# Kernel tuning notes

Measured on AMD Instinct MI355X. Metric: run time of the kernel, lower is better.

Reference implementation:

```python
import jax, jax.numpy as jnp
import numpy as np

B, L, C, S, W, R = 2, 32, 32, 64, 64, 32
MH = 32  # forcing MLP hidden


def _conv3d(x, w, b, pad_hw):
    # x: [B, Cin, L, S, W], w: [Cout, Cin, 1, kh, kw]
    y = jax.lax.conv_general_dilated(
        x, w, window_strides=(1, 1, 1),
        padding=[(0, 0), (pad_hw, pad_hw), (pad_hw, pad_hw)],
        dimension_numbers=('NCDHW', 'OIDHW', 'NCDHW'))
    return y + b[None, :, None, None, None]


def _forward(x, listT, params_log_base, dispersion_mod, fm_W1, fm_b1, fm_W2, fm_b2,
             forcing_scale, U_re, U_im, V_re, V_im, pW_re, pW_im, pb_re, pb_im,
             convr_w, convr_b, convi_w, convi_b, projc_w, projc_b, ln_w, ln_b):
    b, l, c, s, w = x.shape
    r = U_re.shape[-1]
    pad = s // 4
    dt = listT.reshape(b, l, 1, 1, 1)

    # FFT with mirror padding along S
    xp = jnp.pad(x, ((0, 0), (0, 0), (0, 0), (pad, pad), (0, 0)), mode='reflect')
    h = jnp.fft.fft2(xp.astype(jnp.complex64), axes=(-2, -1), norm='ortho')

    # complex channel projection
    proj_W = pW_re + 1j * pW_im
    h = jnp.einsum('blcsw,cd->bldsw', h, proj_W)
    h = h + (pb_re + 1j * pb_im)[None, None, :, None, None]

    # back to spatial, crop pad, re-FFT
    hs = jnp.fft.ifft2(h, axes=(-2, -1), norm='ortho')[..., pad:-pad, :]
    h = jnp.fft.fft2(hs, axes=(-2, -1), norm='ortho')

    U = U_re + 1j * U_im          # [C, S, R]
    V = V_re + 1j * V_im          # [C, W, R]
    # zq[b,l,c,r,q] = sum_{s,w} h * conj(U)[c,s,r] * V[c,w,q]
    zq = jnp.einsum('blcsw,csr,cwq->blcrq', h, jnp.conj(U), V)

    nu_base = jnp.exp(params_log_base[0] + dispersion_mod[0]).reshape(1, 1, c, r, 1)
    th_base = jnp.exp(params_log_base[1] + dispersion_mod[1]).reshape(1, 1, c, r, 1)

    # forcing modulation
    ctx = x.mean(axis=(-2, -1))                       # [B, L, C]
    inp = jnp.concatenate([ctx, dt.reshape(b, l, 1)], axis=-1)
    mid = jnp.tanh(inp @ fm_W1 + fm_b1)
    mod = (mid @ fm_W2 + fm_b2).reshape(b, l, c, r, 2)
    dnu = (forcing_scale * jnp.tanh(mod[..., 0]))[..., None]
    dth = (forcing_scale * jnp.tanh(mod[..., 1]))[..., None]

    nu_t = jnp.maximum(nu_base * dt + dnu, 1e-6)       # [B, L, C, R, 1]
    th_t = th_base * dt + dth
    lamb = jnp.exp(jax.lax.complex(-nu_t, th_t))       # complex [B, L, C, R, 1]

    gamma = jnp.sqrt(jnp.maximum(1.0 - jnp.exp(-2.0 * nu_t), 1e-12))
    x_in = zq * gamma.astype(zq.dtype)                 # [B, L, C, R, R]

    # parallel linear-recurrence scan: z_t = lamb_t * z_{t-1} + x_t
    def comb(a, bb):
        a1, x1 = a
        a2, x2 = bb
        return a1 * a2, a2 * x1 + x2
    _, z_out = jax.lax.associative_scan(comb, (lamb, x_in), axis=1)

    # reconstruct spectral field and inverse FFT
    h_rec = jnp.einsum('blcrq,cwq,csr->blcsw', z_out, jnp.conj(V), U)
    h_sp = jnp.fft.ifft2(h_rec, axes=(-2, -1), norm='ortho')

    xr = jnp.transpose(h_sp.real, (0, 2, 1, 3, 4))     # [B, C, L, S, W]
    xi = jnp.transpose(h_sp.imag, (0, 2, 1, 3, 4))
    hr = _conv3d(xr, convr_w, convr_b, 1)
    hi = _conv3d(xi, convi_w, convi_b, 1)
    hf = _conv3d(jnp.concatenate([hr, hi], axis=1), projc_w, projc_b, 0)
    hf = jnp.transpose(hf, (0, 2, 1, 3, 4))            # [B, L, C, S, W]

    # LayerNorm over [S, W]
    mu = hf.mean(axis=(-2, -1), keepdims=True)
    var = hf.var(axis=(-2, -1), keepdims=True)
    hf = (hf - mu) / jnp.sqrt(var + 1e-5) * ln_w + ln_b

    return x + hf


def setup_inputs() -> dict:
    key = jax.random.key(0)
    ks = jax.random.split(key, 20)
    f32 = jnp.float32
    x = jax.random.normal(ks[0], (B, L, C, S, W), dtype=f32)
    listT = jax.random.uniform(ks[1], (B, L), dtype=f32, minval=0.5, maxval=1.5)

    r_min, r_max = 0.8, 0.99
    u1 = jax.random.uniform(ks[2], (C, R), dtype=f32)
    u2 = jax.random.uniform(ks[3], (C, R), dtype=f32)
    nu_log = jnp.log(-0.5 * jnp.log(u1 * (r_max ** 2 - r_min ** 2) + r_min ** 2))
    theta_log = jnp.log(u2 * (2.0 * np.pi))
    params_log_base = jnp.stack([nu_log, theta_log], axis=0)
    dispersion_mod = jnp.zeros((2, C, R), dtype=f32)

    fm_W1 = jax.random.normal(ks[4], (C + 1, MH), dtype=f32) / np.sqrt(C + 1)
    fm_b1 = jnp.zeros((MH,), dtype=f32)
    fm_W2 = jax.random.normal(ks[5], (MH, C * R * 2), dtype=f32) / np.sqrt(MH)
    fm_b2 = jnp.zeros((C * R * 2,), dtype=f32)
    forcing_scale = jnp.float32(0.1)

    cplx_scale = 1.0 / np.sqrt(2.0)
    U_re = jax.random.normal(ks[6], (C, S, R), dtype=f32) * cplx_scale / np.sqrt(S)
    U_im = jax.random.normal(ks[7], (C, S, R), dtype=f32) * cplx_scale / np.sqrt(S)
    V_re = jax.random.normal(ks[8], (C, W, R), dtype=f32) * cplx_scale / np.sqrt(W)
    V_im = jax.random.normal(ks[9], (C, W, R), dtype=f32) * cplx_scale / np.sqrt(W)
    pW_re = jax.random.normal(ks[10], (C, C), dtype=f32) * cplx_scale / np.sqrt(C)
    pW_im = jax.random.normal(ks[11], (C, C), dtype=f32) * cplx_scale / np.sqrt(C)
    pb_re = jnp.zeros((C,), dtype=f32)
    pb_im = jnp.zeros((C,), dtype=f32)

    convr_w = jax.random.normal(ks[12], (C, C, 1, 3, 3), dtype=f32) * (1.0 / np.sqrt(C * 9))
    convr_b = jnp.zeros((C,), dtype=f32)
    convi_w = jax.random.normal(ks[13], (C, C, 1, 3, 3), dtype=f32) * (1.0 / np.sqrt(C * 9))
    convi_b = jnp.zeros((C,), dtype=f32)
    projc_w = jax.random.normal(ks[14], (C, 2 * C, 1, 1, 1), dtype=f32) * (1.0 / np.sqrt(2 * C))
    projc_b = jnp.zeros((C,), dtype=f32)

    ln_w = jnp.ones((S, W), dtype=f32)
    ln_b = jnp.zeros((S, W), dtype=f32)

    return dict(x=x, listT=listT, params_log_base=params_log_base,
                dispersion_mod=dispersion_mod, fm_W1=fm_W1, fm_b1=fm_b1,
                fm_W2=fm_W2, fm_b2=fm_b2, forcing_scale=forcing_scale,
                U_re=U_re, U_im=U_im, V_re=V_re, V_im=V_im,
                pW_re=pW_re, pW_im=pW_im, pb_re=pb_re, pb_im=pb_im,
                convr_w=convr_w, convr_b=convr_b, convi_w=convi_w, convi_b=convi_b,
                projc_w=projc_w, projc_b=projc_b, ln_w=ln_w, ln_b=ln_b)


def reference(x, listT, params_log_base, dispersion_mod, fm_W1, fm_b1, fm_W2, fm_b2,
              forcing_scale, U_re, U_im, V_re, V_im, pW_re, pW_im, pb_re, pb_im,
              convr_w, convr_b, convi_w, convi_b, projc_w, projc_b, ln_w, ln_b):
    return _forward(x, listT, params_log_base, dispersion_mod, fm_W1, fm_b1, fm_W2,
                    fm_b2, forcing_scale, U_re, U_im, V_re, V_im, pW_re, pW_im,
                    pb_re, pb_im, convr_w, convr_b, convi_w, convi_b, projc_w,
                    projc_b, ln_w, ln_b)
```

## Files before the change

### kernel.cpp

```cpp
#include <hip/hip_runtime.h>


typedef __attribute__((ext_vector_type(8))) short short8;
typedef __attribute__((ext_vector_type(4))) float floatx4;

__device__ __forceinline__ unsigned pack_bf16(float re, float im) {
  unsigned a = __float_as_uint(re), b = __float_as_uint(im);
  a = (a + 0x7FFFu + ((a >> 16) & 1u)) >> 16;
  b = (b + 0x7FFFu + ((b >> 16) & 1u)) >> 16;
  return a | (b << 16);
}
__device__ __forceinline__ unsigned short bf16r(float v) {
  unsigned a = __float_as_uint(v);
  return (unsigned short)((a + 0x7FFFu + ((a >> 16) & 1u)) >> 16);
}

__global__ __launch_bounds__(256) void k_mixprep(
    const float* __restrict__ x, const float* __restrict__ pWr,
    const float* __restrict__ pWi,
    const float* __restrict__ U_re, const float* __restrict__ U_im,
    const float* __restrict__ V_re, const float* __restrict__ V_im,
    const float* __restrict__ projc_w, const float* __restrict__ convr_w,
    const float* __restrict__ convi_w,
    unsigned* __restrict__ hs, float* __restrict__ ctxp,
    unsigned* __restrict__ zqA, unsigned* __restrict__ recA,
    unsigned* __restrict__ recB, unsigned* __restrict__ Wtb) {
  __shared__ __align__(16) char smem[33280];
  const int tid = threadIdx.x;
  if (blockIdx.x < 1024) {
    unsigned* xb_s = (unsigned*)smem;
    float(*red)[16][2] = (float(*)[16][2])(smem + 20480);
    unsigned* outb = (unsigned*)smem;
    const int bl = blockIdx.x >> 4;
    const int seg = blockIdx.x & 15;
    const int pxbase = seg * 256;
    const float* xb = x + (size_t)bl * 131072 + pxbase;
    float csa = 0.f, csb = 0.f;
#pragma unroll
    for (int t = 0; t < 4; ++t) {
      int i = t * 256 + tid;
      int c2 = i & 15, g4 = i >> 4;
      float4 a = *(const float4*)(xb + (2 * c2) * 4096 + g4 * 4);
      float4 b = *(const float4*)(xb + (2 * c2 + 1) * 4096 + g4 * 4);
      csa += a.x + a.y + a.z + a.w;
      csb += b.x + b.y + b.z + b.w;
#pragma unroll
      for (int j = 0; j < 4; ++j) {
        int px = g4 * 4 + j;
        xb_s[px * 20 + (((c2 >> 2) ^ (px & 3)) << 2) + (c2 & 3)] =
            pack_bf16(((const float*)&a)[j], ((const float*)&b)[j]);
      }
    }
    red[tid & 15][tid >> 4][0] = csa;
    red[tid & 15][tid >> 4][1] = csb;
    const int lane = tid & 63, wv = tid >> 6;
    const int qd = lane >> 4, ln = lane & 15;
    short8 arL, aiL, arH, aiH;
#pragma unroll
    for (int j = 0; j < 8; ++j) {
      int ci = qd * 8 + j;
      ((short*)&arL)[j] = (short)bf16r(pWr[ci * 32 + ln]);
      ((short*)&aiL)[j] = (short)bf16r(pWi[ci * 32 + ln]);
      ((short*)&arH)[j] = (short)bf16r(pWr[ci * 32 + 16 + ln]);
      ((short*)&aiH)[j] = (short)bf16r(pWi[ci * 32 + 16 + ln]);
    }
    __syncthreads();
    if (tid < 32) {
      int c2 = tid >> 1, part = tid & 1;
      float s = 0.f;
#pragma unroll
      for (int w = 0; w < 16; ++w) s += red[c2][w][part];
      ctxp[(bl * 16 + seg) * 32 + 2 * c2 + part] = s;
    }
    floatx4 RL[4], IL[4], RH[4], IH[4];
#pragma unroll
    for (int pt = 0; pt < 4; ++pt) {
      int pxt = wv * 4 + pt;
      int pxl = pxt * 16 + ln;
      short8 bfr = *(const short8*)&xb_s[pxl * 20 + ((qd ^ (pxl & 3)) << 2)];
      floatx4 z4 = {0.f, 0.f, 0.f, 0.f};
      RL[pt] = __builtin_amdgcn_mfma_f32_16x16x32_bf16(arL, bfr, z4, 0, 0, 0);
      IL[pt] = __builtin_amdgcn_mfma_f32_16x16x32_bf16(aiL, bfr, z4, 0, 0, 0);
      RH[pt] = __builtin_amdgcn_mfma_f32_16x16x32_bf16(arH, bfr, z4, 0, 0, 0);
      IH[pt] = __builtin_amdgcn_mfma_f32_16x16x32_bf16(aiH, bfr, z4, 0, 0, 0);
    }
    __syncthreads();
#pragma unroll
    for (int pt = 0; pt < 4; ++pt) {
      int px = (wv * 4 + pt) * 16 + ln;
#pragma unroll
      for (int j = 0; j < 4; ++j) {
        outb[(qd * 4 + j) * 260 + px] = pack_bf16(RL[pt][j], IL[pt][j]);
        outb[(16 + qd * 4 + j) * 260 + px] = pack_bf16(RH[pt][j], IH[pt][j]);
      }
    }
    __syncthreads();
    unsigned* ho = hs + (size_t)bl * 131072 + pxbase;
    const int px4 = tid & 63, dg = tid >> 6;
#pragma unroll
    for (int dd = 0; dd < 8; ++dd) {
      int d = dg * 8 + dd;
      uint4 v = *(const uint4*)&outb[d * 260 + px4 * 4];
      *(uint4*)(ho + d * 4096 + px4 * 4) = v;
    }
  } else if (blockIdx.x < 1088) {
    float2* A2 = (float2*)smem;
    float2* tw = (float2*)(smem + 16384);
    const int id = blockIdx.x - 1024;
    const int c = id >> 1, src = id & 1;
    const float* Ar = (src ? V_re : U_re) + c * 2048;
    const float* Ai = (src ? V_im : U_im) + c * 2048;
    if (tid < 64) {
      float sa, ca;
      sincosf((float)tid * 0.09817477042468103f, &sa, &ca);
      tw[tid] = make_float2(ca, sa);
    }
#pragma unroll
    for (int t = 0; t < 8; ++t) {
      int idx = t * 256 + tid;
      A2[idx] = make_float2(Ar[idx], Ai[idx]);
    }
    __syncthreads();
    const int kw = tid >> 2, mg = tid & 3;
    float sr[8] = {0.f, 0.f, 0.f, 0.f, 0.f, 0.f, 0.f, 0.f};
    float si[8] = {0.f, 0.f, 0.f, 0.f, 0.f, 0.f, 0.f, 0.f};
#pragma unroll 4
    for (int n = 0; n < 64; ++n) {
      float2 w = tw[(kw * n) & 63];
      float ws = src ? -w.y : w.y;
#pragma unroll
      for (int t4 = 0; t4 < 4; ++t4) {
        float4 p = *(const float4*)&A2[n * 32 + mg * 8 + t4 * 2];
        sr[2 * t4]     += p.x * w.x - p.y * ws;
        si[2 * t4]     += p.x * ws + p.y * w.x;
        sr[2 * t4 + 1] += p.z * w.x - p.w * ws;
        si[2 * t4 + 1] += p.z * ws + p.w * w.x;
      }
    }
#pragma unroll
    for (int j = 0; j < 8; ++j) {
      float r = sr[j] * 0.125f, i2 = si[j] * 0.125f;
      int m = mg * 8 + j;
      unsigned p_ri  = pack_bf16(r, i2);
      unsigned p_rmi = pack_bf16(r, -i2);
      unsigned p_ir  = pack_bf16(i2, r);
      unsigned p_mir = pack_bf16(-i2, r);
      if (src == 0) {
        zqA[((c * 4 + 2) * 32 + m) * 64 + kw] = p_ri;
        zqA[((c * 4 + 3) * 32 + m) * 64 + kw] = p_mir;
        recA[((c * 2 + 0) * 64 + kw) * 32 + m] = p_rmi;
        recA[((c * 2 + 1) * 64 + kw) * 32 + m] = p_ir;
      } else {
        zqA[((c * 4 + 0) * 32 + m) * 64 + kw] = p_rmi;
        zqA[((c * 4 + 1) * 32 + m) * 64 + kw] = p_ir;
        recB[((c * 2 + 0) * 64 + kw) * 32 + m] = p_ri;
        recB[((c * 2 + 1) * 64 + kw) * 32 + m] = p_mir;
      }
    }
  } else {
    int gid = (blockIdx.x - 1088) * 256 + tid;
    if (gid < 9216) {
      int co = gid / 288;
      int r2 = gid - co * 288;
      int tap = r2 >> 5, ci = r2 & 31;
      float sr = 0.f, si = 0.f;
      for (int m = 0; m < 32; ++m) {
        sr += projc_w[co * 64 + m]      * convr_w[(m * 32 + ci) * 9 + tap];
        si += projc_w[co * 64 + 32 + m] * convi_w[(m * 32 + ci) * 9 + tap];
      }
      Wtb[gid] = pack_bf16(sr, si);
    }
  }
}

__global__ __launch_bounds__(256) void k_zq(
    const unsigned* __restrict__ hs, const short* __restrict__ zqA,
    float2* __restrict__ zq,
    const float* __restrict__ ctxp, const float* __restrict__ listT,
    const float* __restrict__ plb, const float* __restrict__ dmod,
    const float* __restrict__ W1, const float* __restrict__ b1,
    const float* __restrict__ W2, const float* __restrict__ b2,
    const float* __restrict__ fscale,
    float2* __restrict__ lam, float* __restrict__ gam) {
  __shared__ unsigned HsB[4096];
  __shared__ unsigned T2[2048];
  __shared__ float mid_s[32];
  __shared__ float ctxs[32];
  const int tid = threadIdx.x;
  if (blockIdx.x >= 2048) {
    int bl = blockIdx.x - 2048;
    float dt = listT[bl];
    if (tid < 32) {
      float s = 0.f;
#pragma unroll
      for (int sg = 0; sg < 16; ++sg) s += ctxp[(bl * 16 + sg) * 32 + tid];
      ctxs[tid] = s * (1.f / 4096.f);
    }
    __syncthreads();
    if (tid < 32) {
      float a = b1[tid];
      for (int j = 0; j < 32; ++j) a += ctxs[j] * W1[j * 32 + tid];
      a += dt * W1[1024 + tid];
      mid_s[tid] = tanhf(a);
    }
    __syncthreads();
    float fs = fscale[0];
#pragma unroll
    for (int u = 0; u < 4; ++u) {
      int cr = u * 256 + tid;
      int col = cr * 2;
      float m0 = b2[col], m1 = b2[col + 1];
      for (int h = 0; h < 32; ++h) {
        float mh = mid_s[h];
        float2 w2 = *(const float2*)&W2[h * 2048 + col];
        m0 += mh * w2.x;
        m1 += mh * w2.y;
      }
      float dnu = fs * tanhf(m0);
      float dth = fs * tanhf(m1);
      float nub = expf(plb[cr] + dmod[cr]);
      float thb = expf(plb[1024 + cr] + dmod[1024 + cr]);
      float nut = fmaxf(nub * dt + dnu, 1e-6f);
      float tht = thb * dt + dth;
      float e = expf(-nut);
      float sa, ca;
      sincosf(tht, &sa, &ca);
      float g = sqrtf(fmaxf(1.f - expf(-2.f * nut), 1e-12f));
      int o = bl * 1024 + cr;
      lam[o] = make_float2(e * ca, e * sa);
      gam[o] = g;
    }
    return;
  }
  const int blc = blockIdx.x;
  const int c = blc & 31;
  const int lane = tid & 63, wv = tid >> 6;
  const int qd = lane >> 4, ln = lane & 15;
  const int mt = wv >> 1, nth = wv & 1;
  {
    const uint4* hp = (const uint4*)(hs + (size_t)blc * 4096);
#pragma unroll
    for (int it = 0; it < 4; ++it) {
      int i4 = tid + it * 256;
      uint4 v = hp[i4];
      int s = i4 >> 4, w4 = i4 & 15;
      *(uint4*)&HsB[s * 64 + ((w4 ^ (s & 15)) << 2)] = v;
    }
  }
  const short* zA = zqA + (size_t)c * 4 * 32 * 128;
  short8 a1[4], a2[4], a3[4], a4[4];
#pragma unroll
  for (int t = 0; t < 4; ++t) {
    int row = mt * 16 + ln;
    a1[t] = *(const short8*)(zA + (0 * 32 + row) * 128 + t * 32 + qd * 8);
    a2[t] = *(const short8*)(zA + (1 * 32 + row) * 128 + t * 32 + qd * 8);
    a3[t] = *(const short8*)(zA + (2 * 32 + row) * 128 + t * 32 + qd * 8);
    a4[t] = *(const short8*)(zA + (3 * 32 + row) * 128 + t * 32 + qd * 8);
  }
  __syncthreads();
#pragma unroll
  for (int nti = 0; nti < 2; ++nti) {
    int nt = nth * 2 + nti;
    int n = nt * 16 + ln;
    floatx4 accr = {0.f, 0.f, 0.f, 0.f}, acci = {0.f, 0.f, 0.f, 0.f};
#pragma unroll
    for (int t = 0; t < 4; ++t) {
      short8 b = *(const short8*)&HsB[n * 64 + (((4 * t + qd) ^ (n & 15)) << 2)];
      accr = __builtin_amdgcn_mfma_f32_16x16x32_bf16(a1[t], b, accr, 0, 0, 0);
      acci = __builtin_amdgcn_mfma_f32_16x16x32_bf16(a2[t], b, acci, 0, 0, 0);
    }
#pragma unroll
    for (int j = 0; j < 4; ++j) {
      int q = mt * 16 + qd * 4 + j;
      int s = n;
      T2[q * 64 + (((s >> 2) ^ (q & 15)) << 2) + (s & 3)] = pack_bf16(accr[j], acci[j]);
    }
  }
  __syncthreads();
  {
    const int mt2 = wv >> 1, nt2 = wv & 1;
    int n = nt2 * 16 + ln;
    floatx4 zr = {0.f, 0.f, 0.f, 0.f}, zi = {0.f, 0.f, 0.f, 0.f};
#pragma unroll
    for (int t = 0; t < 4; ++t) {
      short8 b = *(const short8*)&T2[n * 64 + (((4 * t + qd) ^ (n & 15)) << 2)];
      zr = __builtin_amdgcn_mfma_f32_16x16x32_bf16(a3[t], b, zr, 0, 0, 0);
      zi = __builtin_amdgcn_mfma_f32_16x16x32_bf16(a4[t], b, zi, 0, 0, 0);
    }
    float2* zo = zq + (size_t)blc * 1024;
#pragma unroll
    for (int j = 0; j < 4; ++j) {
      int r = mt2 * 16 + qd * 4 + j;
      zo[r * 32 + n] = make_float2(zr[j], zi[j]);
    }
  }
}

__global__ __launch_bounds__(256) void k_scan(const float2* __restrict__ lam,
                                              const float* __restrict__ gam,
                                              const float2* __restrict__ zin,
                                              unsigned* __restrict__ zsp,
                                              int zst) {
  __shared__ float2 se[4][64];
  __shared__ float2 pe[4][64];
  __shared__ float2 cr_s[4][64];
  const int bc = blockIdx.x >> 4;
  const int b = bc >> 5, c = bc & 31;
  const int rq0 = (blockIdx.x & 15) * 64;
  const int seg = threadIdx.x >> 6, u = threadIdx.x & 63;
  const int rq = rq0 + u, r = rq >> 5;
  const int t0 = seg * 8;
  float2 s = make_float2(0.f, 0.f), P = make_float2(1.f, 0.f);
  float2 zloc[8], Ps[8];
  float2 v = zin[((size_t)(b * 32 + t0) * 32 + c) * 1024 + rq];
  float2 lm = lam[(b * 32 + t0) * 1024 + c * 32 + r];
  float g = gam[(b * 32 + t0) * 1024 + c * 32 + r];
#pragma unroll
  for (int i = 0; i < 8; ++i) {
    float2 nv, nlm;
    float ng;
    if (i < 7) {
      int t = t0 + i + 1;
      nv = zin[((size_t)(b * 32 + t) * 32 + c) * 1024 + rq];
      nlm = lam[(b * 32 + t) * 1024 + c * 32 + r];
      ng = gam[(b * 32 + t) * 1024 + c * 32 + r];
    }
    float nr = lm.x * s.x - lm.y * s.y + g * v.x;
    float ni = lm.x * s.y + lm.y * s.x + g * v.y;
    s = make_float2(nr, ni);
    float pr = P.x * lm.x - P.y * lm.y;
    float pi = P.x * lm.y + P.y * lm.x;
    P = make_float2(pr, pi);
    zloc[i] = s;
    Ps[i] = P;
    v = nv; lm = nlm; g = ng;
  }
  se[seg][u] = s;
  pe[seg][u] = P;
  __syncthreads();
  if (threadIdx.x < 64) {
    float2 c1 = se[0][u];
    float2 p1 = pe[1][u], s1 = se[1][u];
    float2 c2 = make_float2(s1.x + p1.x * c1.x - p1.y * c1.y,
                            s1.y + p1.x * c1.y + p1.y * c1.x);
    float2 p2 = pe[2][u], s2 = se[2][u];
    float2 c3 = make_float2(s2.x + p2.x * c2.x - p2.y * c2.y,
                            s2.y + p2.x * c2.y + p2.y * c2.x);
    cr_s[0][u] = make_float2(0.f, 0.f);
    cr_s[1][u] = c1;
    cr_s[2][u] = c2;
    cr_s[3][u] = c3;
  }
  __syncthreads();
  float2 cr = cr_s[seg][u];
#pragma unroll
  for (int i = 0; i < 8; ++i) {
    float zr = zloc[i].x + Ps[i].x * cr.x - Ps[i].y * cr.y;
    float zi = zloc[i].y + Ps[i].x * cr.y + Ps[i].y * cr.x;
    size_t idx = ((size_t)(b * 32 + t0 + i) * 32 + c) * 1024 + rq;
    zsp[idx * zst] = pack_bf16(zr, zi);
  }
}

__global__ __launch_bounds__(256) void k_rec(const unsigned* __restrict__ zs,
                                             int zst,
                                             const short* __restrict__ recA,
                                             const short* __restrict__ recB,
                                             unsigned* __restrict__ hsp) {
  __shared__ unsigned zB[1024];
  __shared__ unsigned P[2048];
  const int blc = blockIdx.x;
  const int c = blc & 31;
  const int tid = threadIdx.x;
  const int lane = tid & 63, wv = tid >> 6;
  const int qd = lane >> 4, ln = lane & 15;
  {
    const unsigned* zp = zs + (size_t)blc * 1024 * zst;
#pragma unroll
    for (int it = 0; it < 4; ++it) {
      int i = tid + it * 256;
      unsigned pv = zp[(size_t)i * zst];
      int r = i >> 5, q = i & 31;
      zB[q * 32 + (((r >> 2) ^ (q & 7)) << 2) + (r & 3)] = pv;
    }
  }
  const short* rA = recA + (size_t)c * 2 * 64 * 64;
  short8 a5[2], a6[2];
#pragma unroll
  for (int t = 0; t < 2; ++t) {
    int row = wv * 16 + ln;
    a5[t] = *(const short8*)(rA + (0 * 64 + row) * 64 + t * 32 + qd * 8);
    a6[t] = *(const short8*)(rA + (1 * 64 + row) * 64 + t * 32 + qd * 8);
  }
  __syncthreads();
#pragma unroll
  for (int nt = 0; nt < 2; ++nt) {
    int n = nt * 16 + ln;
    floatx4 pr = {0.f, 0.f, 0.f, 0.f}, pi = {0.f, 0.f, 0.f, 0.f};
#pragma unroll
    for (int t = 0; t < 2; ++t) {
      short8 b = *(const short8*)&zB[n * 32 + (((4 * t + qd) ^ (n & 7)) << 2)];
      pr = __builtin_amdgcn_mfma_f32_16x16x32_bf16(a5[t], b, pr, 0, 0, 0);
      pi = __builtin_amdgcn_mfma_f32_16x16x32_bf16(a6[t], b, pi, 0, 0, 0);
    }
#pragma unroll
    for (int j = 0; j < 4; ++j) {
      int s = wv * 16 + qd * 4 + j;
      int q = n;
      P[s * 32 + (((q >> 2) ^ (s & 7)) << 2) + (q & 3)] = pack_bf16(pr[j], pi[j]);
    }
  }
  __syncthreads();
  const short* rB = recB + (size_t)c * 2 * 64 * 64;
  short8 pa[2];
#pragma unroll
  for (int t = 0; t < 2; ++t) {
    int row = wv * 16 + ln;
    pa[t] = *(const short8*)&P[row * 32 + (((4 * t + qd) ^ (row & 7)) << 2)];
  }
#pragma unroll
  for (int nt = 0; nt < 4; ++nt) {
    int n = nt * 16 + ln;
    floatx4 hr = {0.f, 0.f, 0.f, 0.f}, hi = {0.f, 0.f, 0.f, 0.f};
#pragma unroll
    for (int t = 0; t < 2; ++t) {
      short8 b5 = *(const short8*)(rB + (0 * 64 + n) * 64 + t * 32 + qd * 8);
      short8 b6 = *(const short8*)(rB + (1 * 64 + n) * 64 + t * 32 + qd * 8);
      hr = __builtin_amdgcn_mfma_f32_16x16x32_bf16(pa[t], b5, hr, 0, 0, 0);
      hi = __builtin_amdgcn_mfma_f32_16x16x32_bf16(pa[t], b6, hi, 0, 0, 0);
    }
    unsigned* ho = hsp + (size_t)blc * 4096;
#pragma unroll
    for (int j = 0; j < 4; ++j) {
      int s = wv * 16 + qd * 4 + j;
      ho[s * 64 + n] = pack_bf16(hr[j], hi[j]);
    }
  }
}

__global__ __launch_bounds__(256, 2) void k_conv(
    const unsigned* __restrict__ hsp, const short* __restrict__ Wtb,
    unsigned short* __restrict__ convout, float2* __restrict__ stats) {
  __shared__ unsigned lds_in[6 * 66 * 32];
  const int bl = blockIdx.x >> 4;
  const int slab = blockIdx.x & 15;
  const int y0 = slab * 4;
  const int tid = threadIdx.x;
  for (int i = tid; i < 384; i += 256) {
    int ci = i & 31, j = i >> 5;
    int yi = j >> 1, xi = (j & 1) ? 65 : 0;
    int slot = (ci >> 2) ^ (xi & 7);
    lds_in[(yi * 66 + xi) * 32 + slot * 4 + (ci & 3)] = 0u;
  }
#pragma unroll
  for (int t = 0; t < 12; ++t) {
    int i = t * 256 + tid;
    int ci = i & 31;
    int j = i >> 5;
    int yi = j >> 4, x4 = j & 15;
    int y = y0 + yi - 1;
    uint4 v = make_uint4(0u, 0u, 0u, 0u);
    if ((unsigned)y < 64u)
      v = *(const uint4*)(hsp + (((size_t)bl * 32 + ci) * 64 + y) * 64 + x4 * 4);
    int xb = 1 + x4 * 4;
#pragma unroll
    for (int jj = 0; jj < 4; ++jj) {
      int xi = xb + jj;
      int slot = (ci >> 2) ^ (xi & 7);
      lds_in[(yi * 66 + xi) * 32 + slot * 4 + (ci & 3)] =
          ((const unsigned*)&v)[jj];
    }
  }
  const int lane = tid & 63;
  const int wv = tid >> 6;
  const int co = lane & 15;
  const int qd = lane >> 4;
  short8 bL[18], bH[18];
  {
    const short* wpL = Wtb + (co * 9) * 64 + qd * 8;
    const short* wpH = Wtb + ((co + 16) * 9) * 64 + qd * 8;
#pragma unroll
    for (int tap = 0; tap < 9; ++tap)
#pragma unroll
      for (int kk = 0; kk < 2; ++kk) {
        bL[tap * 2 + kk] = *(const short8*)(wpL + tap * 64 + kk * 32);
        bH[tap * 2 + kk] = *(const short8*)(wpH + tap * 64 + kk * 32);
      }
  }
  __syncthreads();
  float sL = 0.f, s2L = 0.f, sH = 0.f, s2H = 0.f;
  const int x0 = wv * 16;
  const int xl = lane & 15;
  for (int ry = 0; ry < 4; ++ry) {
    floatx4 aL = {0.f, 0.f, 0.f, 0.f}, aH = {0.f, 0.f, 0.f, 0.f};
#pragma unroll
    for (int tap = 0; tap < 9; ++tap) {
      int dy = tap / 3, dx = tap - dy * 3;
      int yi = ry + dy;
      int xi = x0 + xl + dx;
#pragma unroll
      for (int kk = 0; kk < 2; ++kk) {
        int slot = ((kk << 2) | qd) ^ (xi & 7);
        const short8 a =
            *(const short8*)&lds_in[(yi * 66 + xi) * 32 + slot * 4];
        aL = __builtin_amdgcn_mfma_f32_16x16x32_bf16(a, bL[tap * 2 + kk], aL, 0, 0, 0);
        aH = __builtin_amdgcn_mfma_f32_16x16x32_bf16(a, bH[tap * 2 + kk], aH, 0, 0, 0);
      }
    }
    size_t goL = (((size_t)bl * 32 + co) * 64 + (y0 + ry)) * 64 + x0 + qd * 4;
    size_t goH = goL + (size_t)16 * 4096;
    *(uint2*)(convout + goL) =
        make_uint2(pack_bf16(aL[0], aL[1]), pack_bf16(aL[2], aL[3]));
    *(uint2*)(convout + goH) =
        make_uint2(pack_bf16(aH[0], aH[1]), pack_bf16(aH[2], aH[3]));
#pragma unroll
    for (int j = 0; j < 4; ++j) {
      sL += aL[j]; s2L += aL[j] * aL[j];
      sH += aH[j]; s2H += aH[j] * aH[j];
    }
  }
  sL += __shfl_down(sL, 32, 64);  s2L += __shfl_down(s2L, 32, 64);
  sH += __shfl_down(sH, 32, 64);  s2H += __shfl_down(s2H, 32, 64);
  sL += __shfl_down(sL, 16, 64);  s2L += __shfl_down(s2L, 16, 64);
  sH += __shfl_down(sH, 16, 64);  s2H += __shfl_down(s2H, 16, 64);
  if (lane < 16) {
    stats[((size_t)bl * 32 + lane) * 64 + slab * 4 + wv] = make_float2(sL, s2L);
    stats[((size_t)bl * 32 + 16 + lane) * 64 + slab * 4 + wv] =
        make_float2(sH, s2H);
  }
}

__global__ __launch_bounds__(256) void k_ln(
    const unsigned short* __restrict__ convout,
    const float2* __restrict__ stats, const float* __restrict__ x,
    const float* __restrict__ ln_w, const float* __restrict__ ln_b,
    float* __restrict__ out) {
  const int blc = blockIdx.x;
  const int tid = threadIdx.x;
  __shared__ float sh_mu, sh_rs;
  if (tid < 64) {
    float2 v = stats[(size_t)blc * 64 + tid];
    float s = v.x, s2 = v.y;
#pragma unroll
    for (int o = 32; o > 0; o >>= 1) {
      s += __shfl_down(s, o, 64);
      s2 += __shfl_down(s2, o, 64);
    }
    if (tid == 0) {
      float mu = s * (1.f / 4096.f);
      float var = s2 * (1.f / 4096.f) - mu * mu;
      sh_mu = mu;
      sh_rs = rsqrtf(var + 1e-5f);
    }
  }
  __syncthreads();
  float mu = sh_mu, rs = sh_rs;
  const uint2* cp = (const uint2*)(convout + (size_t)blc * 4096);
  const float4* xp = (const float4*)(x + (size_t)blc * 4096);
  const float4* lwp = (const float4*)ln_w;
  const float4* lbp = (const float4*)ln_b;
  float4* op = (float4*)(out + (size_t)blc * 4096);
#pragma unroll
  for (int k = 0; k < 4; ++k) {
    int i = tid + k * 256;
    uint2 cv = cp[i];
    float4 xv = xp[i], lw = lwp[i], lb = lbp[i];
    float c0 = __uint_as_float(cv.x << 16);
    float c1 = __uint_as_float(cv.x & 0xFFFF0000u);
    float c2 = __uint_as_float(cv.y << 16);
    float c3 = __uint_as_float(cv.y & 0xFFFF0000u);
    float4 o;
    o.x = xv.x + (c0 - mu) * rs * lw.x + lb.x;
    o.y = xv.y + (c1 - mu) * rs * lw.y + lb.y;
    o.z = xv.z + (c2 - mu) * rs * lw.z + lb.z;
    o.w = xv.w + (c3 - mu) * rs * lw.w + lb.w;
    op[i] = o;
  }
}

extern "C" void kernel_launch(void* const* d_in, const int* in_sizes, int n_in,
                              void* d_out, int out_size, void* d_ws,
                              size_t ws_size, hipStream_t stream) {
  const float* x       = (const float*)d_in[0];
  const float* listT   = (const float*)d_in[1];
  const float* plb     = (const float*)d_in[2];
  const float* dmod    = (const float*)d_in[3];
  const float* fm_W1   = (const float*)d_in[4];
  const float* fm_b1   = (const float*)d_in[5];
  const float* fm_W2   = (const float*)d_in[6];
  const float* fm_b2   = (const float*)d_in[7];
  const float* fscale  = (const float*)d_in[8];
  const float* U_re    = (const float*)d_in[9];
  const float* U_im    = (const float*)d_in[10];
  const float* V_re    = (const float*)d_in[11];
  const float* V_im    = (const float*)d_in[12];
  const float* pW_re   = (const float*)d_in[13];
  const float* pW_im   = (const float*)d_in[14];
  const float* convr_w = (const float*)d_in[17];
  const float* convi_w = (const float*)d_in[19];
  const float* projc_w = (const float*)d_in[21];
  const float* ln_w    = (const float*)d_in[23];
  const float* ln_b    = (const float*)d_in[24];
  float* out = (float*)d_out;

  float* wsf = (float*)d_ws;
  unsigned* hs  = (unsigned*)wsf;
  unsigned* hsp = (unsigned*)wsf;
  unsigned* zqAp  = (unsigned*)(wsf + 8388608);
  unsigned* recAp = (unsigned*)(wsf + 8388608 + 262144);
  unsigned* recBp = (unsigned*)(wsf + 8388608 + 393216);
  unsigned short* convout = (unsigned short*)(wsf + 8388608);
  float2*   stats = (float2*)(wsf + 12582912);
  float2*   zq  = (float2*)(wsf + 16777216);
  size_t off = 16777216 + 4194304;
  const size_t tail = 238592;
  unsigned* zs;
  int zst;
  size_t off2;
  if (ws_size >= (off + 2097152 + tail) * 4) {
    zs = (unsigned*)(wsf + off); zst = 1; off2 = off + 2097152;
  } else {
    zs = (unsigned*)zq; zst = 2; off2 = off;
  }
  float2*   lam  = (float2*)(wsf + off2);
  float*    gam  = wsf + off2 + 131072;
  float*    ctxp = wsf + off2 + 196608;
  unsigned* Wtb  = (unsigned*)(wsf + off2 + 229376);

  k_mixprep<<<1124, 256, 0, stream>>>(x, pW_re, pW_im, U_re, U_im, V_re, V_im,
                                      projc_w, convr_w, convi_w, hs, ctxp,
                                      zqAp, recAp, recBp, Wtb);
  k_zq<<<2112, 256, 0, stream>>>(hs, (const short*)zqAp, zq, ctxp, listT, plb,
                                 dmod, fm_W1, fm_b1, fm_W2, fm_b2, fscale,
                                 lam, gam);
  k_scan<<<1024, 256, 0, stream>>>(lam, gam, zq, zs, zst);
  k_rec<<<2048, 256, 0, stream>>>(zs, zst, (const short*)recAp,
                                  (const short*)recBp, hsp);
  k_conv<<<1024, 256, 0, stream>>>(hsp, (const short*)Wtb, convout, stats);
  k_ln<<<2048, 256, 0, stream>>>(convout, stats, x, ln_w, ln_b, out);
}
```

Before: 240.2 us.

## Fuse zq projection, time scan and reconstruction into one persistent per-(b,c) kernel

Replaces the separate k_zq, k_scan and k_rec kernels with a single k_mid kernel. Each of its 64 blocks of 512 threads owns one (batch, channel) pair and steps through time two frames per round, keeping the recurrence state in registers and the intermediates in LDS. This removes the global round-trips of the zq and scanned-z buffers and two kernel launches. The forcing-MLP and lambda/gamma computation moves into dedicated k_mixprep blocks that recompute the spatial mean directly from x, which re-reads x. The trade-off is a serial 16-round loop with several barriers per round, running on only 64 blocks, which leaves most CUs idle during that phase.

```diff
diff --git a/kernel.cpp b/kernel.cpp
--- a/kernel.cpp
+++ b/kernel.cpp
@@ -22,28 +22,89 @@
     const float* __restrict__ V_re, const float* __restrict__ V_im,
     const float* __restrict__ projc_w, const float* __restrict__ convr_w,
     const float* __restrict__ convi_w,
-    unsigned* __restrict__ hs, float* __restrict__ ctxp,
-    unsigned* __restrict__ zqA, unsigned* __restrict__ recA,
-    unsigned* __restrict__ recB, unsigned* __restrict__ Wtb) {
+    const float* __restrict__ listT, const float* __restrict__ plb,
+    const float* __restrict__ dmod, const float* __restrict__ W1,
+    const float* __restrict__ b1, const float* __restrict__ W2,
+    const float* __restrict__ b2, const float* __restrict__ fscale,
+    unsigned* __restrict__ hs, unsigned* __restrict__ zqA,
+    unsigned* __restrict__ recA, unsigned* __restrict__ recB,
+    unsigned* __restrict__ Wtb, float2* __restrict__ lam,
+    float* __restrict__ gam) {
   __shared__ __align__(16) char smem[33280];
   const int tid = threadIdx.x;
-  if (blockIdx.x < 1024) {
+  const int bid = blockIdx.x;
+  if (bid < 64) {
+    float* cred = (float*)smem;
+    float* ctxs = cred + 256;
+    float* mid_s = ctxs + 32;
+    const int bl = bid;
+    {
+      int c = tid >> 3, sub = tid & 7;
+      const float4* xb = (const float4*)(x + (size_t)bl * 131072 + c * 4096);
+      float s = 0.f;
+#pragma unroll 8
+      for (int m = 0; m < 128; ++m) {
+        float4 v = xb[sub + m * 8];
+        s += v.x + v.y + v.z + v.w;
+      }
+      cred[c * 8 + sub] = s;
+    }
+    __syncthreads();
+    if (tid < 32) {
+      float t = 0.f;
+#pragma unroll
+      for (int k = 0; k < 8; ++k) t += cred[tid * 8 + k];
+      ctxs[tid] = t * (1.f / 4096.f);
+    }
+    __syncthreads();
+    float dt = listT[bl];
+    if (tid < 32) {
+      float a = b1[tid];
+      for (int j = 0; j < 32; ++j) a += ctxs[j] * W1[j * 32 + tid];
+      a += dt * W1[1024 + tid];
+      mid_s[tid] = tanhf(a);
+    }
+    __syncthreads();
+    float fs = fscale[0];
+#pragma unroll
+    for (int u = 0; u < 4; ++u) {
+      int cr = u * 256 + tid;
+      int col = cr * 2;
+      float m0 = b2[col], m1 = b2[col + 1];
+      for (int h = 0; h < 32; ++h) {
+        float mh = mid_s[h];
+        float2 w2 = *(const float2*)&W2[h * 2048 + col];
+        m0 += mh * w2.x;
+        m1 += mh * w2.y;
+      }
+      float dnu = fs * tanhf(m0);
+      float dth = fs * tanhf(m1);
+      float nub = expf(plb[cr] + dmod[cr]);
+      float thb = expf(plb[1024 + cr] + dmod[1024 + cr]);
+      float nut = fmaxf(nub * dt + dnu, 1e-6f);
+      float tht = thb * dt + dth;
+      float e = expf(-nut);
+      float sa, ca;
+      sincosf(tht, &sa, &ca);
+      float g = sqrtf(fmaxf(1.f - expf(-2.f * nut), 1e-12f));
+      int o = bl * 1024 + cr;
+      lam[o] = make_float2(e * ca, e * sa);
+      gam[o] = g;
+    }
+  } else if (bid < 1088) {
     unsigned* xb_s = (unsigned*)smem;
-    float(*red)[16][2] = (float(*)[16][2])(smem + 20480);
     unsigned* outb = (unsigned*)smem;
-    const int bl = blockIdx.x >> 4;
-    const int seg = blockIdx.x & 15;
+    const int wk = bid - 64;
+    const int bl = wk >> 4;
+    const int seg = wk & 15;
     const int pxbase = seg * 256;
     const float* xb = x + (size_t)bl * 131072 + pxbase;
-    float csa = 0.f, csb = 0.f;
 #pragma unroll
     for (int t = 0; t < 4; ++t) {
       int i = t * 256 + tid;
       int c2 = i & 15, g4 = i >> 4;
       float4 a = *(const float4*)(xb + (2 * c2) * 4096 + g4 * 4);
       float4 b = *(const float4*)(xb + (2 * c2 + 1) * 4096 + g4 * 4);
-      csa += a.x + a.y + a.z + a.w;
-      csb += b.x + b.y + b.z + b.w;
 #pragma unroll
       for (int j = 0; j < 4; ++j) {
         int px = g4 * 4 + j;
@@ -51,8 +112,6 @@
             pack_bf16(((const float*)&a)[j], ((const float*)&b)[j]);
       }
     }
-    red[tid & 15][tid >> 4][0] = csa;
-    red[tid & 15][tid >> 4][1] = csb;
     const int lane = tid & 63, wv = tid >> 6;
     const int qd = lane >> 4, ln = lane & 15;
     short8 arL, aiL, arH, aiH;
@@ -65,13 +124,6 @@
       ((short*)&aiH)[j] = (short)bf16r(pWi[ci * 32 + 16 + ln]);
     }
     __syncthreads();
-    if (tid < 32) {
-      int c2 = tid >> 1, part = tid & 1;
-      float s = 0.f;
-#pragma unroll
-      for (int w = 0; w < 16; ++w) s += red[c2][w][part];
-      ctxp[(bl * 16 + seg) * 32 + 2 * c2 + part] = s;
-    }
     floatx4 RL[4], IL[4], RH[4], IH[4];
 #pragma unroll
     for (int pt = 0; pt < 4; ++pt) {
@@ -103,10 +155,10 @@
       uint4 v = *(const uint4*)&outb[d * 260 + px4 * 4];
       *(uint4*)(ho + d * 4096 + px4 * 4) = v;
     }
-  } else if (blockIdx.x < 1088) {
+  } else if (bid < 1152) {
     float2* A2 = (float2*)smem;
     float2* tw = (float2*)(smem + 16384);
-    const int id = blockIdx.x - 1024;
+    const int id = bid - 1088;
     const int c = id >> 1, src = id & 1;
     const float* Ar = (src ? V_re : U_re) + c * 2048;
     const float* Ai = (src ? V_im : U_im) + c * 2048;
@@ -130,11 +182,11 @@
       float ws = src ? -w.y : w.y;
 #pragma unroll
       for (int t4 = 0; t4 < 4; ++t4) {
-        float4 p = *(const float4*)&A2[n * 32 + mg * 8 + t4 * 2];
-        sr[2 * t4]     += p.x * w.x - p.y * ws;
-        si[2 * t4]     += p.x * ws + p.y * w.x;
-        sr[2 * t4 + 1] += p.z * w.x - p.w * ws;
-        si[2 * t4 + 1] += p.z * ws + p.w * w.x;
+        float4 q = *(const float4*)&A2[n * 32 + mg * 8 + t4 * 2];
+        sr[2 * t4]     += q.x * w.x - q.y * ws;
+        si[2 * t4]     += q.x * ws + q.y * w.x;
+        sr[2 * t4 + 1] += q.z * w.x - q.w * ws;
+        si[2 * t4 + 1] += q.z * ws + q.w * w.x;
       }
     }
 #pragma unroll
@@ -158,7 +210,7 @@
       }
     }
   } else {
-    int gid = (blockIdx.x - 1088) * 256 + tid;
+    int gid = (bid - 1152) * 256 + tid;
     if (gid < 9216) {
       int co = gid / 288;
       int r2 = gid - co * 288;
@@ -173,80 +225,25 @@
   }
 }
 
-__global__ __launch_bounds__(256) void k_zq(
+__global__ __launch_bounds__(512, 2) void k_mid(
     const unsigned* __restrict__ hs, const short* __restrict__ zqA,
-    float2* __restrict__ zq,
-    const float* __restrict__ ctxp, const float* __restrict__ listT,
-    const float* __restrict__ plb, const float* __restrict__ dmod,
-    const float* __restrict__ W1, const float* __restrict__ b1,
-    const float* __restrict__ W2, const float* __restrict__ b2,
-    const float* __restrict__ fscale,
-    float2* __restrict__ lam, float* __restrict__ gam) {
-  __shared__ unsigned HsB[4096];
-  __shared__ unsigned T2[2048];
-  __shared__ float mid_s[32];
-  __shared__ float ctxs[32];
+    const short* __restrict__ recA, const short* __restrict__ recB,
+    const float2* __restrict__ lam, const float* __restrict__ gam,
+    unsigned* __restrict__ hsp) {
+  __shared__ __align__(16) char smem[61440];
+  float2* lam_s = (float2*)smem;
+  float*  gam_s = (float*)(smem + 8192);
+  unsigned* HsB = (unsigned*)(smem + 12288);
+  float2* zqt   = (float2*)(smem + 12288);
+  unsigned* zB  = (unsigned*)(smem + 28672);
+  unsigned* T2P = (unsigned*)(smem + 45056);
   const int tid = threadIdx.x;
-  if (blockIdx.x >= 2048) {
-    int bl = blockIdx.x - 2048;
-    float dt = listT[bl];
-    if (tid < 32) {
-      float s = 0.f;
-#pragma unroll
-      for (int sg = 0; sg < 16; ++sg) s += ctxp[(bl * 16 + sg) * 32 + tid];
-      ctxs[tid] = s * (1.f / 4096.f);
-    }
-    __syncthreads();
-    if (tid < 32) {
-      float a = b1[tid];
-      for (int j = 0; j < 32; ++j) a += ctxs[j] * W1[j * 32 + tid];
-      a += dt * W1[1024 + tid];
-      mid_s[tid] = tanhf(a);
-    }
-    __syncthreads();
-    float fs = fscale[0];
-#pragma unroll
-    for (int u = 0; u < 4; ++u) {
-      int cr = u * 256 + tid;
-      int col = cr * 2;
-      float m0 = b2[col], m1 = b2[col + 1];
-      for (int h = 0; h < 32; ++h) {
-        float mh = mid_s[h];
-        float2 w2 = *(const float2*)&W2[h * 2048 + col];
-        m0 += mh * w2.x;
-        m1 += mh * w2.y;
-      }
-      float dnu = fs * tanhf(m0);
-      float dth = fs * tanhf(m1);
-      float nub = expf(plb[cr] + dmod[cr]);
-      float thb = expf(plb[1024 + cr] + dmod[1024 + cr]);
-      float nut = fmaxf(nub * dt + dnu, 1e-6f);
-      float tht = thb * dt + dth;
-      float e = expf(-nut);
-      float sa, ca;
-      sincosf(tht, &sa, &ca);
-      float g = sqrtf(fmaxf(1.f - expf(-2.f * nut), 1e-12f));
-      int o = bl * 1024 + cr;
-      lam[o] = make_float2(e * ca, e * sa);
-      gam[o] = g;
-    }
-    return;
-  }
-  const int blc = blockIdx.x;
-  const int c = blc & 31;
+  const int b = blockIdx.x >> 5, c = blockIdx.x & 31;
   const int lane = tid & 63, wv = tid >> 6;
+  const int grp = wv >> 2, wvg = wv & 3;
+  const int tg = tid & 255;
   const int qd = lane >> 4, ln = lane & 15;
-  const int mt = wv >> 1, nth = wv & 1;
-  {
-    const uint4* hp = (const uint4*)(hs + (size_t)blc * 4096);
-#pragma unroll
-    for (int it = 0; it < 4; ++it) {
-      int i4 = tid + it * 256;
-      uint4 v = hp[i4];
-      int s = i4 >> 4, w4 = i4 & 15;
-      *(uint4*)&HsB[s * 64 + ((w4 ^ (s & 15)) << 2)] = v;
-    }
-  }
+  const int mt = wvg >> 1, nth = wvg & 1;
   const short* zA = zqA + (size_t)c * 4 * 32 * 128;
   short8 a1[4], a2[4], a3[4], a4[4];
 #pragma unroll
@@ -257,184 +254,162 @@
     a3[t] = *(const short8*)(zA + (2 * 32 + row) * 128 + t * 32 + qd * 8);
     a4[t] = *(const short8*)(zA + (3 * 32 + row) * 128 + t * 32 + qd * 8);
   }
-  __syncthreads();
-#pragma unroll
-  for (int nti = 0; nti < 2; ++nti) {
-    int nt = nth * 2 + nti;
-    int n = nt * 16 + ln;
-    floatx4 accr = {0.f, 0.f, 0.f, 0.f}, acci = {0.f, 0.f, 0.f, 0.f};
-#pragma unroll
-    for (int t = 0; t < 4; ++t) {
-      short8 b = *(const short8*)&HsB[n * 64 + (((4 * t + qd) ^ (n & 15)) << 2)];
-      accr = __builtin_amdgcn_mfma_f32_16x16x32_bf16(a1[t], b, accr, 0, 0, 0);
-      acci = __builtin_amdgcn_mfma_f32_16x16x32_bf16(a2[t], b, acci, 0, 0, 0);
-    }
-#pragma unroll
-    for (int j = 0; j < 4; ++j) {
-      int q = mt * 16 + qd * 4 + j;
-      int s = n;
-      T2[q * 64 + (((s >> 2) ^ (q & 15)) << 2) + (s & 3)] = pack_bf16(accr[j], acci[j]);
-    }
-  }
-  __syncthreads();
-  {
-    const int mt2 = wv >> 1, nt2 = wv & 1;
-    int n = nt2 * 16 + ln;
-    floatx4 zr = {0.f, 0.f, 0.f, 0.f}, zi = {0.f, 0.f, 0.f, 0.f};
-#pragma unroll
-    for (int t = 0; t < 4; ++t) {
-      short8 b = *(const short8*)&T2[n * 64 + (((4 * t + qd) ^ (n & 15)) << 2)];
-      zr = __builtin_amdgcn_mfma_f32_16x16x32_bf16(a3[t], b, zr, 0, 0, 0);
-      zi = __builtin_amdgcn_mfma_f32_16x16x32_bf16(a4[t], b, zi, 0, 0, 0);
-    }
-    float2* zo = zq + (size_t)blc * 1024;
-#pragma unroll
-    for (int j = 0; j < 4; ++j) {
-      int r = mt2 * 16 + qd * 4 + j;
-      zo[r * 32 + n] = make_float2(zr[j], zi[j]);
-    }
-  }
-}
-
-__global__ __launch_bounds__(256) void k_scan(const float2* __restrict__ lam,
-                                              const float* __restrict__ gam,
-                                              const float2* __restrict__ zin,
-                                              unsigned* __restrict__ zsp,
-                                              int zst) {
-  __shared__ float2 se[4][64];
-  __shared__ float2 pe[4][64];
-  __shared__ float2 cr_s[4][64];
-  const int bc = blockIdx.x >> 4;
-  const int b = bc >> 5, c = bc & 31;
-  const int rq0 = (blockIdx.x & 15) * 64;
-  const int seg = threadIdx.x >> 6, u = threadIdx.x & 63;
-  const int rq = rq0 + u, r = rq >> 5;
-  const int t0 = seg * 8;
-  float2 s = make_float2(0.f, 0.f), P = make_float2(1.f, 0.f);
-  float2 zloc[8], Ps[8];
-  float2 v = zin[((size_t)(b * 32 + t0) * 32 + c) * 1024 + rq];
-  float2 lm = lam[(b * 32 + t0) * 1024 + c * 32 + r];
-  float g = gam[(b * 32 + t0) * 1024 + c * 32 + r];
-#pragma unroll
-  for (int i = 0; i < 8; ++i) {
-    float2 nv, nlm;
-    float ng;
-    if (i < 7) {
-      int t = t0 + i + 1;
-      nv = zin[((size_t)(b * 32 + t) * 32 + c) * 1024 + rq];
-      nlm = lam[(b * 32 + t) * 1024 + c * 32 + r];
-      ng = gam[(b * 32 + t) * 1024 + c * 32 + r];
-    }
-    float nr = lm.x * s.x - lm.y * s.y + g * v.x;
-    float ni = lm.x * s.y + lm.y * s.x + g * v.y;
-    s = make_float2(nr, ni);
-    float pr = P.x * lm.x - P.y * lm.y;
-    float pi = P.x * lm.y + P.y * lm.x;
-    P = make_float2(pr, pi);
-    zloc[i] = s;
-    Ps[i] = P;
-    v = nv; lm = nlm; g = ng;
-  }
-  se[seg][u] = s;
-  pe[seg][u] = P;
-  __syncthreads();
-  if (threadIdx.x < 64) {
-    float2 c1 = se[0][u];
-    float2 p1 = pe[1][u], s1 = se[1][u];
-    float2 c2 = make_float2(s1.x + p1.x * c1.x - p1.y * c1.y,
-                            s1.y + p1.x * c1.y + p1.y * c1.x);
-    float2 p2 = pe[2][u], s2 = se[2][u];
-    float2 c3 = make_float2(s2.x + p2.x * c2.x - p2.y * c2.y,
-                            s2.y + p2.x * c2.y + p2.y * c2.x);
-    cr_s[0][u] = make_float2(0.f, 0.f);
-    cr_s[1][u] = c1;
-    cr_s[2][u] = c2;
-    cr_s[3][u] = c3;
-  }
-  __syncthreads();
-  float2 cr = cr_s[seg][u];
-#pragma unroll
-  for (int i = 0; i < 8; ++i) {
-    float zr = zloc[i].x + Ps[i].x * cr.x - Ps[i].y * cr.y;
-    float zi = zloc[i].y + Ps[i].x * cr.y + Ps[i].y * cr.x;
-    size_t idx = ((size_t)(b * 32 + t0 + i) * 32 + c) * 1024 + rq;
-    zsp[idx * zst] = pack_bf16(zr, zi);
-  }
-}
-
-__global__ __launch_bounds__(256) void k_rec(const unsigned* __restrict__ zs,
-                                             int zst,
-                                             const short* __restrict__ recA,
-                                             const short* __restrict__ recB,
-                                             unsigned* __restrict__ hsp) {
-  __shared__ unsigned zB[1024];
-  __shared__ unsigned P[2048];
-  const int blc = blockIdx.x;
-  const int c = blc & 31;
-  const int tid = threadIdx.x;
-  const int lane = tid & 63, wv = tid >> 6;
-  const int qd = lane >> 4, ln = lane & 15;
-  {
-    const unsigned* zp = zs + (size_t)blc * 1024 * zst;
-#pragma unroll
-    for (int it = 0; it < 4; ++it) {
-      int i = tid + it * 256;
-      unsigned pv = zp[(size_t)i * zst];
-      int r = i >> 5, q = i & 31;
-      zB[q * 32 + (((r >> 2) ^ (q & 7)) << 2) + (r & 3)] = pv;
-    }
-  }
   const short* rA = recA + (size_t)c * 2 * 64 * 64;
   short8 a5[2], a6[2];
 #pragma unroll
   for (int t = 0; t < 2; ++t) {
-    int row = wv * 16 + ln;
+    int row = wvg * 16 + ln;
     a5[t] = *(const short8*)(rA + (0 * 64 + row) * 64 + t * 32 + qd * 8);
     a6[t] = *(const short8*)(rA + (1 * 64 + row) * 64 + t * 32 + qd * 8);
   }
+  const short* rB = recB + (size_t)c * 2 * 64 * 64;
+  for (int idx = tid; idx < 1024; idx += 512) {
+    int l = idx >> 5, r = idx & 31;
+    lam_s[idx] = lam[(b * 32 + l) * 1024 + c * 32 + r];
+    gam_s[idx] = gam[(b * 32 + l) * 1024 + c * 32 + r];
+  }
+  {
+    const uint4* hp =
+        (const uint4*)(hs + (size_t)((b * 32 + grp) * 32 + c) * 4096);
+#pragma unroll
+    for (int it = 0; it < 4; ++it) {
+      int i4 = tg + it * 256;
+      uint4 v = hp[i4];
+      int s = i4 >> 4, w4 = i4 & 15;
+      *(uint4*)&HsB[grp * 4096 + s * 64 + ((w4 ^ (s & 15)) << 2)] = v;
+    }
+  }
+  float2 st[4];
+#pragma unroll
+  for (int j = 0; j < 4; ++j) st[j] = make_float2(0.f, 0.f);
   __syncthreads();
-#pragma unroll
-  for (int nt = 0; nt < 2; ++nt) {
-    int n = nt * 16 + ln;
-    floatx4 pr = {0.f, 0.f, 0.f, 0.f}, pi = {0.f, 0.f, 0.f, 0.f};
-#pragma unroll
-    for (int t = 0; t < 2; ++t) {
-      short8 b = *(const short8*)&zB[n * 32 + (((4 * t + qd) ^ (n & 7)) << 2)];
-      pr = __builtin_amdgcn_mfma_f32_16x16x32_bf16(a5[t], b, pr, 0, 0, 0);
-      pi = __builtin_amdgcn_mfma_f32_16x16x32_bf16(a6[t], b, pi, 0, 0, 0);
-    }
-#pragma unroll
-    for (int j = 0; j < 4; ++j) {
-      int s = wv * 16 + qd * 4 + j;
-      int q = n;
-      P[s * 32 + (((q >> 2) ^ (s & 7)) << 2) + (q & 3)] = pack_bf16(pr[j], pi[j]);
-    }
-  }
-  __syncthreads();
-  const short* rB = recB + (size_t)c * 2 * 64 * 64;
-  short8 pa[2];
-#pragma unroll
-  for (int t = 0; t < 2; ++t) {
-    int row = wv * 16 + ln;
-    pa[t] = *(const short8*)&P[row * 32 + (((4 * t + qd) ^ (row & 7)) << 2)];
-  }
-#pragma unroll
-  for (int nt = 0; nt < 4; ++nt) {
-    int n = nt * 16 + ln;
-    floatx4 hr = {0.f, 0.f, 0.f, 0.f}, hi = {0.f, 0.f, 0.f, 0.f};
-#pragma unroll
-    for (int t = 0; t < 2; ++t) {
-      short8 b5 = *(const short8*)(rB + (0 * 64 + n) * 64 + t * 32 + qd * 8);
-      short8 b6 = *(const short8*)(rB + (1 * 64 + n) * 64 + t * 32 + qd * 8);
-      hr = __builtin_amdgcn_mfma_f32_16x16x32_bf16(pa[t], b5, hr, 0, 0, 0);
-      hi = __builtin_amdgcn_mfma_f32_16x16x32_bf16(pa[t], b6, hi, 0, 0, 0);
-    }
-    unsigned* ho = hsp + (size_t)blc * 4096;
-#pragma unroll
-    for (int j = 0; j < 4; ++j) {
-      int s = wv * 16 + qd * 4 + j;
-      ho[s * 64 + n] = pack_bf16(hr[j], hi[j]);
-    }
+  for (int round = 0; round < 16; ++round) {
+    const int l0 = round * 2;
+    const int blc = (b * 32 + l0 + grp) * 32 + c;
+#pragma unroll
+    for (int nti = 0; nti < 2; ++nti) {
+      int nt = nth * 2 + nti;
+      int n = nt * 16 + ln;
+      floatx4 accr = {0.f, 0.f, 0.f, 0.f}, acci = {0.f, 0.f, 0.f, 0.f};
+#pragma unroll
+      for (int t = 0; t < 4; ++t) {
+        short8 bb = *(const short8*)&HsB[grp * 4096 + n * 64 +
+                                         (((4 * t + qd) ^ (n & 15)) << 2)];
+        accr = __builtin_amdgcn_mfma_f32_16x16x32_bf16(a1[t], bb, accr, 0, 0, 0);
+        acci = __builtin_amdgcn_mfma_f32_16x16x32_bf16(a2[t], bb, acci, 0, 0, 0);
+      }
+#pragma unroll
+      for (int j = 0; j < 4; ++j) {
+        int q = mt * 16 + qd * 4 + j;
+        int s = n;
+        T2P[grp * 2048 + q * 64 + (((s >> 2) ^ (q & 15)) << 2) + (s & 3)] =
+            pack_bf16(accr[j], acci[j]);
+      }
+    }
+    __syncthreads();
+    {
+      int n = nth * 16 + ln;
+      floatx4 zr = {0.f, 0.f, 0.f, 0.f}, zi = {0.f, 0.f, 0.f, 0.f};
+#pragma unroll
+      for (int t = 0; t < 4; ++t) {
+        short8 bb = *(const short8*)&T2P[grp * 2048 + n * 64 +
+                                         (((4 * t + qd) ^ (n & 15)) << 2)];
+        zr = __builtin_amdgcn_mfma_f32_16x16x32_bf16(a3[t], bb, zr, 0, 0, 0);
+        zi = __builtin_amdgcn_mfma_f32_16x16x32_bf16(a4[t], bb, zi, 0, 0, 0);
+      }
+#pragma unroll
+      for (int j = 0; j < 4; ++j) {
+        int r = mt * 16 + qd * 4 + j;
+        zqt[grp * 1024 + r * 32 + n] = make_float2(zr[j], zi[j]);
+      }
+    }
+    __syncthreads();
+    {
+      int q = nth * 16 + ln;
+#pragma unroll
+      for (int j = 0; j < 4; ++j) {
+        int r = mt * 16 + qd * 4 + j;
+        float2 lm = lam_s[l0 * 32 + r];
+        float g = gam_s[l0 * 32 + r];
+        float2 v = zqt[r * 32 + q];
+        float nr = lm.x * st[j].x - lm.y * st[j].y + g * v.x;
+        float ni = lm.x * st[j].y + lm.y * st[j].x + g * v.y;
+        st[j] = make_float2(nr, ni);
+        unsigned pk = pack_bf16(nr, ni);
+        lm = lam_s[(l0 + 1) * 32 + r];
+        g = gam_s[(l0 + 1) * 32 + r];
+        v = zqt[1024 + r * 32 + q];
+        nr = lm.x * st[j].x - lm.y * st[j].y + g * v.x;
+        ni = lm.x * st[j].y + lm.y * st[j].x + g * v.y;
+        st[j] = make_float2(nr, ni);
+        if (grp) pk = pack_bf16(nr, ni);
+        zB[grp * 1024 + q * 32 + (((r >> 2) ^ (q & 7)) << 2) + (r & 3)] = pk;
+      }
+    }
+    __syncthreads();
+#pragma unroll
+    for (int nt = 0; nt < 2; ++nt) {
+      int n = nt * 16 + ln;
+      floatx4 pr = {0.f, 0.f, 0.f, 0.f}, pi = {0.f, 0.f, 0.f, 0.f};
+#pragma unroll
+      for (int t = 0; t < 2; ++t) {
+        short8 bb = *(const short8*)&zB[grp * 1024 + n * 32 +
+                                        (((4 * t + qd) ^ (n & 7)) << 2)];
+        pr = __builtin_amdgcn_mfma_f32_16x16x32_bf16(a5[t], bb, pr, 0, 0, 0);
+        pi = __builtin_amdgcn_mfma_f32_16x16x32_bf16(a6[t], bb, pi, 0, 0, 0);
+      }
+#pragma unroll
+      for (int j = 0; j < 4; ++j) {
+        int s = wvg * 16 + qd * 4 + j;
+        int q = n;
+        T2P[grp * 2048 + s * 32 + (((q >> 2) ^ (s & 7)) << 2) + (q & 3)] =
+            pack_bf16(pr[j], pi[j]);
+      }
+    }
+    __syncthreads();
+    uint4 sv[4];
+    const bool more = (round < 15);
+    if (more) {
+      const uint4* hp = (const uint4*)(
+          hs + (size_t)((b * 32 + l0 + 2 + grp) * 32 + c) * 4096);
+#pragma unroll
+      for (int it = 0; it < 4; ++it) sv[it] = hp[tg + it * 256];
+    }
+    {
+      short8 pa[2];
+      int row = wvg * 16 + ln;
+#pragma unroll
+      for (int t = 0; t < 2; ++t)
+        pa[t] = *(const short8*)&T2P[grp * 2048 + row * 32 +
+                                     (((4 * t + qd) ^ (row & 7)) << 2)];
+      unsigned* ho = hsp + (size_t)blc * 4096;
+#pragma unroll
+      for (int nt = 0; nt < 4; ++nt) {
+        int n = nt * 16 + ln;
+        floatx4 hr = {0.f, 0.f, 0.f, 0.f}, hi = {0.f, 0.f, 0.f, 0.f};
+#pragma unroll
+        for (int t = 0; t < 2; ++t) {
+          short8 b5 = *(const short8*)(rB + (0 * 64 + n) * 64 + t * 32 + qd * 8);
+          short8 b6 = *(const short8*)(rB + (1 * 64 + n) * 64 + t * 32 + qd * 8);
+          hr = __builtin_amdgcn_mfma_f32_16x16x32_bf16(pa[t], b5, hr, 0, 0, 0);
+          hi = __builtin_amdgcn_mfma_f32_16x16x32_bf16(pa[t], b6, hi, 0, 0, 0);
+        }
+#pragma unroll
+        for (int j = 0; j < 4; ++j) {
+          int s = wvg * 16 + qd * 4 + j;
+          ho[s * 64 + n] = pack_bf16(hr[j], hi[j]);
+        }
+      }
+    }
+    if (more) {
+#pragma unroll
+      for (int it = 0; it < 4; ++it) {
+        int i4 = tg + it * 256;
+        int s = i4 >> 4, w4 = i4 & 15;
+        *(uint4*)&HsB[grp * 4096 + s * 64 + ((w4 ^ (s & 15)) << 2)] = sv[it];
+      }
+    }
+    __syncthreads();
   }
 }
 
@@ -604,38 +579,23 @@
   float* out = (float*)d_out;
 
   float* wsf = (float*)d_ws;
-  unsigned* hs  = (unsigned*)wsf;
-  unsigned* hsp = (unsigned*)wsf;
-  unsigned* zqAp  = (unsigned*)(wsf + 8388608);
-  unsigned* recAp = (unsigned*)(wsf + 8388608 + 262144);
-  unsigned* recBp = (unsigned*)(wsf + 8388608 + 393216);
-  unsigned short* convout = (unsigned short*)(wsf + 8388608);
-  float2*   stats = (float2*)(wsf + 12582912);
-  float2*   zq  = (float2*)(wsf + 16777216);
-  size_t off = 16777216 + 4194304;
-  const size_t tail = 238592;
-  unsigned* zs;
-  int zst;
-  size_t off2;
-  if (ws_size >= (off + 2097152 + tail) * 4) {
-    zs = (unsigned*)(wsf + off); zst = 1; off2 = off + 2097152;
-  } else {
-    zs = (unsigned*)zq; zst = 2; off2 = off;
-  }
-  float2*   lam  = (float2*)(wsf + off2);
-  float*    gam  = wsf + off2 + 131072;
-  float*    ctxp = wsf + off2 + 196608;
-  unsigned* Wtb  = (unsigned*)(wsf + off2 + 229376);
-
-  k_mixprep<<<1124, 256, 0, stream>>>(x, pW_re, pW_im, U_re, U_im, V_re, V_im,
-                                      projc_w, convr_w, convi_w, hs, ctxp,
-                                      zqAp, recAp, recBp, Wtb);
-  k_zq<<<2112, 256, 0, stream>>>(hs, (const short*)zqAp, zq, ctxp, listT, plb,
-                                 dmod, fm_W1, fm_b1, fm_W2, fm_b2, fscale,
-                                 lam, gam);
-  k_scan<<<1024, 256, 0, stream>>>(lam, gam, zq, zs, zst);
-  k_rec<<<2048, 256, 0, stream>>>(zs, zst, (const short*)recAp,
-                                  (const short*)recBp, hsp);
+  unsigned* hs   = (unsigned*)wsf;
+  unsigned* hsp  = (unsigned*)(wsf + 8388608);
+  unsigned* zqAp = (unsigned*)(wsf + 16777216);
+  unsigned* recAp = (unsigned*)(wsf + 17039360);
+  unsigned* recBp = (unsigned*)(wsf + 17170432);
+  unsigned short* convout = (unsigned short*)(wsf + 17301504);
+  float2*   stats = (float2*)(wsf + 25690112);
+  float2*   lam   = (float2*)(wsf + 25952256);
+  float*    gam   = wsf + 26083328;
+  unsigned* Wtb   = (unsigned*)(wsf + 26148864);
+
+  k_mixprep<<<1188, 256, 0, stream>>>(x, pW_re, pW_im, U_re, U_im, V_re, V_im,
+                                      projc_w, convr_w, convi_w, listT, plb,
+                                      dmod, fm_W1, fm_b1, fm_W2, fm_b2, fscale,
+                                      hs, zqAp, recAp, recBp, Wtb, lam, gam);
+  k_mid<<<64, 512, 0, stream>>>(hs, (const short*)zqAp, (const short*)recAp,
+                                (const short*)recBp, lam, gam, hsp);
   k_conv<<<1024, 256, 0, stream>>>(hsp, (const short*)Wtb, convout, stats);
   k_ln<<<2048, 256, 0, stream>>>(convout, stats, x, ln_w, ln_b, out);
 }
```

Result: slower. 264.7 us (+10.2%).
